# Kernel optimization log

Measured on AMD Instinct MI355X. Metric: run time of the kernel, lower is better.

The kernel has to match this reference:

```python
import jax, jax.numpy as jnp
import numpy as np

N_HEADS = 16
KEY_SIZE = 64
N_INPUTS = 512
B, T = 128, 200


def setup_inputs() -> dict:
    key = jax.random.key(0)
    ks = jax.random.split(key, 6)
    s = 0.02
    return {
        "x": jax.random.normal(ks[0], (B, T, N_INPUTS), dtype=jnp.float32),
        "Wq": jax.random.normal(ks[1], (N_INPUTS, N_HEADS * KEY_SIZE), dtype=jnp.float32) * s,
        "bq": jnp.zeros((N_HEADS * KEY_SIZE,), dtype=jnp.float32),
        "Wk": jax.random.normal(ks[2], (N_INPUTS, N_HEADS * KEY_SIZE), dtype=jnp.float32) * s,
        "bk": jnp.zeros((N_HEADS * KEY_SIZE,), dtype=jnp.float32),
        "Wv": jax.random.normal(ks[3], (N_INPUTS, N_HEADS * N_INPUTS), dtype=jnp.float32) * s,
        "bv": jnp.zeros((N_HEADS * N_INPUTS,), dtype=jnp.float32),
        "Wp": jax.random.normal(ks[4], (N_HEADS * N_INPUTS, N_INPUTS), dtype=jnp.float32) * s,
        "bp": jnp.zeros((N_INPUTS,), dtype=jnp.float32),
    }


def reference(x, Wq, bq, Wk, bk, Wv, bv, Wp, bp):
    Bx, Tx, C = x.shape
    H, K = N_HEADS, KEY_SIZE
    # projections -> (B, H, T, d)
    q = (x @ Wq + bq).reshape(Bx, Tx, H, K).transpose(0, 2, 1, 3)
    k = (x @ Wk + bk).reshape(Bx, Tx, H, K).transpose(0, 2, 1, 3)
    v = (x @ Wv + bv).reshape(Bx, Tx, H, C).transpose(0, 2, 1, 3)
    scale = 1.0 / np.sqrt(K).astype(np.float32)
    scores = jnp.einsum("bhtk,bhsk->bhts", q, k) * scale  # (B,H,T,T)
    causal = jnp.tril(jnp.ones((Tx, Tx), dtype=bool))
    scores = jnp.where(causal[None, None], scores, -jnp.inf)
    att = jax.nn.softmax(scores, axis=-1)  # dropout p=0.0 (eval)
    y = jnp.einsum("bhts,bhsc->bhtc", att, v)  # (B,H,T,C)
    y = y.transpose(0, 2, 1, 3).reshape(Bx, Tx, H * C)
    return (y @ Wp + bp, att)
```

## Files before the change

kernel.cpp:

```cpp
#include <hip/hip_runtime.h>

typedef unsigned short u16;
typedef short v8s __attribute__((ext_vector_type(8)));
typedef float v4f __attribute__((ext_vector_type(4)));

#define DEV __device__ __forceinline__

constexpr int BATCH = 128;
constexpr int T = 200;
constexpr int C = 512;
constexpr int H = 16;
constexpr int BT = BATCH * T;
constexpr int TP = 208;
constexpr int TPK = 224;
constexpr int HK = 1024;
constexpr int HC = 8192;
constexpr float SCALE = 0.125f;

DEV u16 f2b(float x) {
  union { float f; unsigned u; } v; v.f = x;
  unsigned r = v.u + 0x7fffu + ((v.u >> 16) & 1u);
  return (u16)(r >> 16);
}

__global__ void cast_bf16_kernel(const float* __restrict__ in, u16* __restrict__ out, long n4) {
  long i = (long)blockIdx.x * blockDim.x + threadIdx.x;
  long stride = (long)gridDim.x * blockDim.x;
  for (; i < n4; i += stride) {
    float4 v = *(const float4*)(in + i * 4);
    uint2 o;
    o.x = (unsigned)f2b(v.x) | ((unsigned)f2b(v.y) << 16);
    o.y = (unsigned)f2b(v.z) | ((unsigned)f2b(v.w) << 16);
    *(uint2*)(out + i * 4) = o;
  }
}

__global__ void transpose_cast_kernel(const float* __restrict__ in, u16* __restrict__ out,
                                      int R, int Cc, int Rpad, long inBatch, long outBatch) {
  __shared__ float tile[32][33];
  int b = blockIdx.z;
  int c0 = blockIdx.x * 32, r0 = blockIdx.y * 32;
  int tx = threadIdx.x, ty = threadIdx.y;
  const float* ib = in + (long)b * inBatch;
  u16* ob = out + (long)b * outBatch;
  for (int i = ty; i < 32; i += 8) {
    int r = r0 + i, c = c0 + tx;
    tile[i][tx] = (r < R && c < Cc) ? ib[(long)r * Cc + c] : 0.f;
  }
  __syncthreads();
  for (int i = ty; i < 32; i += 8) {
    int c = c0 + i, r = r0 + tx;
    if (c < Cc && r < Rpad) ob[(long)c * Rpad + r] = f2b(tile[tx][i]);
  }
}

__global__ void cvec_init_kernel(const float* __restrict__ bp, float* __restrict__ cvec) {
  int j = threadIdx.x + blockIdx.x * 256;
  if (j < C) cvec[j] = bp[j];
}
__global__ void cvec_kernel(const float* __restrict__ bv, const float* __restrict__ Wp,
                            float* __restrict__ cvec) {
  int j = blockIdx.x * 256 + threadIdx.x;
  int hc0 = blockIdx.y * 256;
  float acc = 0.f;
  for (int i = 0; i < 256; i++) {
    int hc = hc0 + i;
    acc += bv[hc] * Wp[(long)hc * C + j];
  }
  atomicAdd(&cvec[j], acc);
}

template<bool OUT_BF16, bool BIAS, bool ACCUM, bool Y2T>
__global__ __launch_bounds__(256) void gemm_nt_kernel(
    const u16* __restrict__ A, long lda, long strideA,
    const u16* __restrict__ Bt, long ldb, long strideB,
    void* __restrict__ Dp, long ldd, long strideD,
    const float* __restrict__ bias, int K, int ntN) {
  __shared__ __align__(16) u16 As[128 * 64];
  __shared__ __align__(16) u16 Bs[128 * 64];
  int bt = blockIdx.y;
  int tn = blockIdx.x % ntN, tm = blockIdx.x / ntN;
  const u16* Ab = A + (long)bt * strideA + (long)tm * 128 * lda;
  const u16* Bb = Bt + (long)bt * strideB + (long)tn * 128 * ldb;
  int tid = threadIdx.x;
  int lane = tid & 63, wave = tid >> 6;
  int r15 = lane & 15, kg = lane >> 4;
  int wm = (wave & 1) * 64, wn = (wave >> 1) * 64;
  v4f acc[4][4] = {};
  for (int kt = 0; kt < K; kt += 64) {
    uint4 va[4], vb[4];
    #pragma unroll
    for (int i = 0; i < 4; i++) {
      int c = i * 256 + tid;
      long row = c >> 3; int c8 = (c & 7) * 8;
      va[i] = *(const uint4*)(Ab + row * lda + kt + c8);
      vb[i] = *(const uint4*)(Bb + row * ldb + kt + c8);
    }
    __syncthreads();
    #pragma unroll
    for (int i = 0; i < 4; i++) {
      int c = i * 256 + tid;
      *(uint4*)(As + c * 8) = va[i];
      *(uint4*)(Bs + c * 8) = vb[i];
    }
    __syncthreads();
    #pragma unroll
    for (int ks = 0; ks < 2; ks++) {
      v8s af[4], bf_[4];
      int ko = ks * 32 + kg * 8;
      #pragma unroll
      for (int mi = 0; mi < 4; mi++) af[mi] = *(const v8s*)(As + (wm + mi * 16 + r15) * 64 + ko);
      #pragma unroll
      for (int ni = 0; ni < 4; ni++) bf_[ni] = *(const v8s*)(Bs + (wn + ni * 16 + r15) * 64 + ko);
      #pragma unroll
      for (int mi = 0; mi < 4; mi++)
        #pragma unroll
        for (int ni = 0; ni < 4; ni++)
          acc[mi][ni] = __builtin_amdgcn_mfma_f32_16x16x32_bf16(af[mi], bf_[ni], acc[mi][ni], 0, 0, 0);
    }
    __syncthreads();
  }
  #pragma unroll
  for (int mi = 0; mi < 4; mi++) {
    #pragma unroll
    for (int ni = 0; ni < 4; ni++) {
      int colg = tn * 128 + wn + ni * 16 + r15;
      float bb = BIAS ? bias[colg] : 0.f;
      #pragma unroll
      for (int r = 0; r < 4; r++) {
        long rowg = (long)tm * 128 + wm + mi * 16 + kg * 4 + r;
        float v = acc[mi][ni][r] + bb;
        if (Y2T) {
          int b2 = colg / T; int ss = colg - b2 * T;
          ((u16*)Dp)[((long)b2 * HC + rowg) * TPK + ss] = f2b(v);
        } else {
          long off = (long)bt * strideD + rowg * ldd + colg;
          if (OUT_BF16)      ((u16*)Dp)[off] = f2b(v);
          else if (ACCUM)    ((float*)Dp)[off] += v;
          else               ((float*)Dp)[off] = v;
        }
      }
    }
  }
}

__global__ __launch_bounds__(256) void attn_kernel(
    const u16* __restrict__ qb, const u16* __restrict__ kb, float* __restrict__ att) {
  __shared__ __align__(16) u16 Qs[TP * 64];
  __shared__ __align__(16) u16 Ks[TP * 64];
  int bh = blockIdx.x;
  int b = bh >> 4, h = bh & 15;
  int tid = threadIdx.x;
  const u16* qg = qb + (long)b * T * HK + h * 64;
  const u16* kg_ = kb + (long)b * T * HK + h * 64;
  for (int c = tid; c < TP * 8; c += 256) {
    long row = c >> 3; int c8 = (c & 7) * 8;
    long srow = row < T ? row : (T - 1);
    *(uint4*)(Qs + c * 8) = *(const uint4*)(qg + srow * HK + c8);
    *(uint4*)(Ks + c * 8) = *(const uint4*)(kg_ + srow * HK + c8);
  }
  __syncthreads();
  int lane = tid & 63, wave = tid >> 6;
  int r15 = lane & 15, kg4 = lane >> 4;
  float* attb = att + (long)bh * T * T;
  for (int tt = wave; tt < 13; tt += 4) {
    v8s aq0 = *(const v8s*)(Qs + (tt * 16 + r15) * 64 + kg4 * 8);
    v8s aq1 = *(const v8s*)(Qs + (tt * 16 + r15) * 64 + 32 + kg4 * 8);
    float sc[13][4];
    #pragma unroll
    for (int j = 0; j < 13; j++) {
      if (j <= tt) {
        v8s bk0 = *(const v8s*)(Ks + (j * 16 + r15) * 64 + kg4 * 8);
        v8s bk1 = *(const v8s*)(Ks + (j * 16 + r15) * 64 + 32 + kg4 * 8);
        v4f a_ = {};
        a_ = __builtin_amdgcn_mfma_f32_16x16x32_bf16(aq0, bk0, a_, 0, 0, 0);
        a_ = __builtin_amdgcn_mfma_f32_16x16x32_bf16(aq1, bk1, a_, 0, 0, 0);
        #pragma unroll
        for (int r = 0; r < 4; r++) {
          int t_ = tt * 16 + kg4 * 4 + r;
          int s_ = j * 16 + r15;
          sc[j][r] = (s_ <= t_) ? a_[r] * SCALE : -__builtin_inff();
        }
      } else {
        #pragma unroll
        for (int r = 0; r < 4; r++) sc[j][r] = -__builtin_inff();
      }
    }
    float sm[4];
    #pragma unroll
    for (int r = 0; r < 4; r++) {
      float m = sc[0][r];
      #pragma unroll
      for (int j = 1; j < 13; j++) m = fmaxf(m, sc[j][r]);
      #pragma unroll
      for (int off = 1; off < 16; off <<= 1) m = fmaxf(m, __shfl_xor(m, off));
      float s = 0.f;
      #pragma unroll
      for (int j = 0; j < 13; j++) { float p = __expf(sc[j][r] - m); sc[j][r] = p; s += p; }
      #pragma unroll
      for (int off = 1; off < 16; off <<= 1) s += __shfl_xor(s, off);
      sm[r] = 1.f / s;
    }
    #pragma unroll
    for (int j = 0; j < 13; j++) {
      int s_ = j * 16 + r15;
      if (s_ < T) {
        #pragma unroll
        for (int r = 0; r < 4; r++) {
          int t_ = tt * 16 + kg4 * 4 + r;
          if (t_ < T) attb[(long)t_ * T + s_] = sc[j][r] * sm[r];
        }
      }
    }
  }
}

__global__ __launch_bounds__(256) void out_kernel(
    const float* __restrict__ att, const u16* __restrict__ y2t,
    const float* __restrict__ cvec, float* __restrict__ out) {
  __shared__ __align__(16) u16 As_[128 * 32];
  __shared__ __align__(16) u16 Bs_[128 * 32];
  int bx = blockIdx.x;
  int mt = bx >> 2, tn = bx & 3;
  int b = blockIdx.y;
  int t0 = mt * 128;
  const float* ab = att + (long)b * H * T * T;
  const u16* yb = y2t + (long)b * HC * TPK;
  int tid = threadIdx.x;
  int lane = tid & 63, wave = tid >> 6;
  int r15 = lane & 15, kg4 = lane >> 4;
  int wm = (wave & 1) * 64, wn = (wave >> 1) * 64;
  int arow = tid >> 1, ac = (tid & 1) * 16;
  v4f acc[4][4] = {};
  int nsc = (t0 == 0) ? 4 : 7;
  for (int h = 0; h < H; h++) {
    const float* ah = ab + (long)h * T * T;
    const u16* yh = yb + (long)(h * C + tn * 128) * TPK;
    for (int sc = 0; sc < nsc; sc++) {
      int s0 = sc * 32;
      int t_ = t0 + arow;
      __align__(16) u16 ta[16];
      #pragma unroll
      for (int e = 0; e < 16; e++) {
        int s_ = s0 + ac + e;
        float v = 0.f;
        if (t_ < T && s_ < T) v = ah[(long)t_ * T + s_];
        ta[e] = f2b(v);
      }
      uint4 bv0 = *(const uint4*)(yh + (long)arow * TPK + s0 + ac);
      uint4 bv1 = *(const uint4*)(yh + (long)arow * TPK + s0 + ac + 8);
      __syncthreads();
      *(uint4*)(As_ + arow * 32 + ac) = *(uint4*)ta;
      *(uint4*)(As_ + arow * 32 + ac + 8) = *(uint4*)(ta + 8);
      *(uint4*)(Bs_ + arow * 32 + ac) = bv0;
      *(uint4*)(Bs_ + arow * 32 + ac + 8) = bv1;
      __syncthreads();
      int ko = kg4 * 8;
      v8s af[4], bf_[4];
      #pragma unroll
      for (int mi = 0; mi < 4; mi++) af[mi] = *(const v8s*)(As_ + (wm + mi * 16 + r15) * 32 + ko);
      #pragma unroll
      for (int ni = 0; ni < 4; ni++) bf_[ni] = *(const v8s*)(Bs_ + (wn + ni * 16 + r15) * 32 + ko);
      #pragma unroll
      for (int mi = 0; mi < 4; mi++)
        #pragma unroll
        for (int ni = 0; ni < 4; ni++)
          acc[mi][ni] = __builtin_amdgcn_mfma_f32_16x16x32_bf16(af[mi], bf_[ni], acc[mi][ni], 0, 0, 0);
      __syncthreads();
    }
  }
  #pragma unroll
  for (int mi = 0; mi < 4; mi++) {
    #pragma unroll
    for (int ni = 0; ni < 4; ni++) {
      int colg = tn * 128 + wn + ni * 16 + r15;
      float bb = cvec[colg];
      #pragma unroll
      for (int r = 0; r < 4; r++) {
        int t_ = t0 + wm + mi * 16 + kg4 * 4 + r;
        if (t_ < T) out[((long)b * T + t_) * C + colg] = acc[mi][ni][r] + bb;
      }
    }
  }
}

extern "C" void kernel_launch(void* const* d_in, const int* in_sizes, int n_in,
                              void* d_out, int out_size, void* d_ws, size_t ws_size,
                              hipStream_t stream) {
  const float* x  = (const float*)d_in[0];
  const float* Wq = (const float*)d_in[1];
  const float* bq = (const float*)d_in[2];
  const float* Wk = (const float*)d_in[3];
  const float* bk = (const float*)d_in[4];
  const float* Wv = (const float*)d_in[5];
  const float* bv = (const float*)d_in[6];
  const float* Wp = (const float*)d_in[7];
  const float* bp = (const float*)d_in[8];
  float* out = (float*)d_out;
  float* att = out + (long)BT * C;

  char* w = (char*)d_ws;
  auto alloc = [&](size_t bytes) -> char* {
    char* p = w; w += (bytes + 255) & ~(size_t)255; return p;
  };
  u16* xb  = (u16*)alloc((size_t)BT * C * 2);
  u16* qb  = (u16*)alloc((size_t)BT * HK * 2);
  u16* kb  = (u16*)alloc((size_t)BT * HK * 2);
  u16* wqT = (u16*)alloc((size_t)HK * C * 2);
  u16* wkT = (u16*)alloc((size_t)HK * C * 2);
  u16* w2n = (u16*)alloc((size_t)HC * C * 2);
  float* cv = (float*)alloc(C * 4);
  char* scratch0 = w;
  u16* wvb = (u16*)alloc((size_t)C * HC * 2);
  u16* wpT = (u16*)alloc((size_t)HC * C * 2);
  u16* y2t = (u16*)scratch0;
  size_t rem = ws_size > (size_t)(scratch0 - (char*)d_ws)
             ? ws_size - (size_t)(scratch0 - (char*)d_ws) : 0;
  int nbc = 128;
  while (nbc > 16 && (size_t)nbc * HC * TPK * 2 > rem) nbc >>= 1;

  cast_bf16_kernel<<<2048, 256, 0, stream>>>(x, xb, (long)BT * C / 4);
  cast_bf16_kernel<<<2048, 256, 0, stream>>>(Wv, wvb, (long)C * HC / 4);
  dim3 tb(32, 8);
  transpose_cast_kernel<<<dim3(HK / 32, C / 32, 1), tb, 0, stream>>>(Wq, wqT, C, HK, C, 0, 0);
  transpose_cast_kernel<<<dim3(HK / 32, C / 32, 1), tb, 0, stream>>>(Wk, wkT, C, HK, C, 0, 0);
  transpose_cast_kernel<<<dim3(C / 32, HC / 32, 1), tb, 0, stream>>>(Wp, wpT, HC, C, HC, 0, 0);
  cvec_init_kernel<<<2, 256, 0, stream>>>(bp, cv);
  cvec_kernel<<<dim3(2, 32), 256, 0, stream>>>(bv, Wp, cv);
  gemm_nt_kernel<true, true, false, false><<<dim3(200 * 8, 1), 256, 0, stream>>>(
      xb, C, 0, wqT, C, 0, qb, HK, 0, bq, C, 8);
  gemm_nt_kernel<true, true, false, false><<<dim3(200 * 8, 1), 256, 0, stream>>>(
      xb, C, 0, wkT, C, 0, kb, HK, 0, bk, C, 8);
  gemm_nt_kernel<true, false, false, false><<<dim3(16, H), 256, 0, stream>>>(
      wpT, HC, C, wvb, HC, C, w2n, C, (long)C * C, nullptr, C, 4);
  attn_kernel<<<dim3(BATCH * H), 256, 0, stream>>>(qb, kb, att);
  for (int b0 = 0; b0 < BATCH; b0 += nbc) {
    int ntn = nbc * T / 128;
    gemm_nt_kernel<false, false, false, true><<<dim3(64 * ntn, 1), 256, 0, stream>>>(
        w2n, C, 0, xb + (long)b0 * T * C, C, 0, y2t, 0, 0, nullptr, C, ntn);
    out_kernel<<<dim3(8, nbc), 256, 0, stream>>>(
        att + (long)b0 * H * T * T, y2t, cv, out + (long)b0 * T * C);
  }
}
```

Before: 2.513 ms.

## Swizzle GEMM LDS, remap workgroups across XCDs, stage Y2T epilogue through LDS

The GEMM kernel now uses an XOR-swizzled LDS layout to avoid bank conflicts on MFMA fragment reads. It remaps block indices so consecutive tiles land on the same XCD, which should improve L2 reuse. The Y2T epilogue first transposes results through shared memory so global stores become coalesced 32-bit writes instead of scattered 16-bit ones. out_kernel is launched on a 1D grid with a similar XCD-aware mapping. The block remap assumes the grid size divides by 8, and the paired stores assume ss is even and stays within the batch row.

```diff
diff --git a/kernel.cpp b/kernel.cpp
--- a/kernel.cpp
+++ b/kernel.cpp
@@ -70,6 +70,8 @@
   atomicAdd(&cvec[j], acc);
 }
 
+DEV int lsw(int row, int chunk) { return row * 64 + ((chunk ^ (row & 7)) << 3); }
+
 template<bool OUT_BF16, bool BIAS, bool ACCUM, bool Y2T>
 __global__ __launch_bounds__(256) void gemm_nt_kernel(
     const u16* __restrict__ A, long lda, long strideA,
@@ -79,7 +81,10 @@
   __shared__ __align__(16) u16 As[128 * 64];
   __shared__ __align__(16) u16 Bs[128 * 64];
   int bt = blockIdx.y;
-  int tn = blockIdx.x % ntN, tm = blockIdx.x / ntN;
+  int nwg = gridDim.x;
+  int orig = blockIdx.x;
+  int bxs = (orig & 7) * (nwg >> 3) + (orig >> 3);
+  int tn = bxs % ntN, tm = bxs / ntN;
   const u16* Ab = A + (long)bt * strideA + (long)tm * 128 * lda;
   const u16* Bb = Bt + (long)bt * strideB + (long)tn * 128 * ldb;
   int tid = threadIdx.x;
@@ -100,18 +105,19 @@
     #pragma unroll
     for (int i = 0; i < 4; i++) {
       int c = i * 256 + tid;
-      *(uint4*)(As + c * 8) = va[i];
-      *(uint4*)(Bs + c * 8) = vb[i];
+      int row = c >> 3, chunk = c & 7;
+      *(uint4*)(As + lsw(row, chunk)) = va[i];
+      *(uint4*)(Bs + lsw(row, chunk)) = vb[i];
     }
     __syncthreads();
     #pragma unroll
     for (int ks = 0; ks < 2; ks++) {
       v8s af[4], bf_[4];
-      int ko = ks * 32 + kg * 8;
-      #pragma unroll
-      for (int mi = 0; mi < 4; mi++) af[mi] = *(const v8s*)(As + (wm + mi * 16 + r15) * 64 + ko);
-      #pragma unroll
-      for (int ni = 0; ni < 4; ni++) bf_[ni] = *(const v8s*)(Bs + (wn + ni * 16 + r15) * 64 + ko);
+      int chunk = ks * 4 + kg;
+      #pragma unroll
+      for (int mi = 0; mi < 4; mi++) af[mi] = *(const v8s*)(As + lsw(wm + mi * 16 + r15, chunk));
+      #pragma unroll
+      for (int ni = 0; ni < 4; ni++) bf_[ni] = *(const v8s*)(Bs + lsw(wn + ni * 16 + r15, chunk));
       #pragma unroll
       for (int mi = 0; mi < 4; mi++)
         #pragma unroll
@@ -120,21 +126,44 @@
     }
     __syncthreads();
   }
-  #pragma unroll
-  for (int mi = 0; mi < 4; mi++) {
-    #pragma unroll
-    for (int ni = 0; ni < 4; ni++) {
-      int colg = tn * 128 + wn + ni * 16 + r15;
-      float bb = BIAS ? bias[colg] : 0.f;
-      #pragma unroll
-      for (int r = 0; r < 4; r++) {
-        long rowg = (long)tm * 128 + wm + mi * 16 + kg * 4 + r;
-        float v = acc[mi][ni][r] + bb;
-        if (Y2T) {
-          int b2 = colg / T; int ss = colg - b2 * T;
-          ((u16*)Dp)[((long)b2 * HC + rowg) * TPK + ss] = f2b(v);
-        } else {
+  if constexpr (Y2T) {
+    #pragma unroll
+    for (int mi = 0; mi < 4; mi++) {
+      #pragma unroll
+      for (int ni = 0; ni < 4; ni++) {
+        int col = wn + ni * 16 + r15;
+        #pragma unroll
+        for (int r = 0; r < 4; r++) {
+          int row = wm + mi * 16 + kg * 4 + r;
+          u16* Trow = (row < 64 ? As : Bs) + (row & 63) * 128;
+          Trow[col] = f2b(acc[mi][ni][r]);
+        }
+      }
+    }
+    __syncthreads();
+    int n0 = tn * 128;
+    for (int it = 0; it < 32; it++) {
+      int row = wave * 32 + it;
+      const u16* Trow = (row < 64 ? As : Bs) + (row & 63) * 128;
+      unsigned d = *(const unsigned*)(Trow + lane * 2);
+      int colg = n0 + lane * 2;
+      int b2 = colg / T;
+      int ss = colg - b2 * T;
+      long rowg = (long)tm * 128 + row;
+      *(unsigned*)((u16*)Dp + ((long)b2 * HC + rowg) * TPK + ss) = d;
+    }
+  } else {
+    #pragma unroll
+    for (int mi = 0; mi < 4; mi++) {
+      #pragma unroll
+      for (int ni = 0; ni < 4; ni++) {
+        int colg = tn * 128 + wn + ni * 16 + r15;
+        float bb = BIAS ? bias[colg] : 0.f;
+        #pragma unroll
+        for (int r = 0; r < 4; r++) {
+          long rowg = (long)tm * 128 + wm + mi * 16 + kg * 4 + r;
           long off = (long)bt * strideD + rowg * ldd + colg;
+          float v = acc[mi][ni][r] + bb;
           if (OUT_BF16)      ((u16*)Dp)[off] = f2b(v);
           else if (ACCUM)    ((float*)Dp)[off] += v;
           else               ((float*)Dp)[off] = v;
@@ -220,9 +249,13 @@
     const float* __restrict__ cvec, float* __restrict__ out) {
   __shared__ __align__(16) u16 As_[128 * 32];
   __shared__ __align__(16) u16 Bs_[128 * 32];
-  int bx = blockIdx.x;
-  int mt = bx >> 2, tn = bx & 3;
-  int b = blockIdx.y;
+  int g = blockIdx.x;
+  int rr = g & 7;
+  int tq = g >> 3;
+  int tn = tq & 3;
+  int idx = (tq >> 2) * 8 + rr;
+  int b = idx >> 1;
+  int mt = idx & 1;
   int t0 = mt * 128;
   const float* ab = att + (long)b * H * T * T;
   const u16* yb = y2t + (long)b * HC * TPK;
@@ -338,7 +371,7 @@
     int ntn = nbc * T / 128;
     gemm_nt_kernel<false, false, false, true><<<dim3(64 * ntn, 1), 256, 0, stream>>>(
         w2n, C, 0, xb + (long)b0 * T * C, C, 0, y2t, 0, 0, nullptr, C, ntn);
-    out_kernel<<<dim3(8, nbc), 256, 0, stream>>>(
+    out_kernel<<<dim3(8 * nbc), 256, 0, stream>>>(
         att + (long)b0 * H * T * T, y2t, cv, out + (long)b0 * T * C);
   }
 }
```

After: 2.472 ms. No clear change (-1.6%).
